# Kernel optimization log

Hardware: AMD Instinct MI355X
Metric: run time of the kernel (lower is better)

The kernel has to match this reference:

```python
import jax, jax.numpy as jnp
import numpy as np
from jax import lax

B, S, D, H = 512, 1024, 24, 64


def setup_inputs() -> dict:
    key = jax.random.key(0)
    ks = jax.random.split(key, 7)
    x = jax.random.normal(ks[0], (B, S, D), dtype=jnp.float32)
    t = jax.random.randint(ks[1], (B,), 0, S, dtype=jnp.int64)
    # Keras GRUCell params (reset_after=True -> bias has shape [2, 3H])
    W = jax.random.normal(ks[2], (D, 3 * H), dtype=jnp.float32) * 0.05   # input kernel
    U = jax.random.normal(ks[3], (H, 3 * H), dtype=jnp.float32) * 0.05   # recurrent kernel
    b = jax.random.normal(ks[4], (2, 3 * H), dtype=jnp.float32) * 0.05   # [input_bias, recurrent_bias]
    Wd = jax.random.normal(ks[5], (H, 1), dtype=jnp.float32) * 0.05      # dense kernel
    bd = jnp.zeros((1,), dtype=jnp.float32)                              # dense bias
    return {"x": x, "t": t, "W": W, "U": U, "b": b, "Wd": Wd, "bd": bd}


def _gru_masked(x, t, W, U, b):
    Bq, Sq, _ = x.shape
    Hq = U.shape[0]
    # prefix mask: True where step index < length (tf.sequence_mask)
    mask = jnp.arange(Sq)[None, :] < t[:, None]          # (B, S) bool
    x_proj = jnp.einsum('bsd,dk->bsk', x, W) + b[0]      # (B, S, 3H) precomputed input gates

    def step(h, inp):
        xp, m = inp                                      # xp: (B, 3H), m: (B,)
        hp = h @ U + b[1]                                # (B, 3H)
        xz, xr, xh = jnp.split(xp, 3, axis=-1)
        hz, hr, hh = jnp.split(hp, 3, axis=-1)
        z = jax.nn.sigmoid(xz + hz)
        r = jax.nn.sigmoid(xr + hr)
        c = jnp.tanh(xh + r * hh)                        # reset_after=True formulation
        h_new = z * h + (1.0 - z) * c
        h_new = jnp.where(m[:, None], h_new, h)          # masked step: carry state/output
        return h_new, h_new

    h0 = jnp.zeros((Bq, Hq), x.dtype)
    xs = jnp.swapaxes(x_proj, 0, 1)                      # (S, B, 3H)
    ms = jnp.swapaxes(mask, 0, 1)                        # (S, B)
    _, hs = lax.scan(step, h0, (xs, ms))
    return jnp.swapaxes(hs, 0, 1)                        # (B, S, H)


def reference(x, t, W, U, b, Wd, bd):
    rnn_out = _gru_masked(x, t, W, U, b)                 # (B, S, H)
    logit = rnn_out @ Wd + bd                            # (B, S, 1)
    return jax.nn.sigmoid(logit)
```

## Files before the change

kernel.cpp:

```cpp
#include <hip/hip_runtime.h>
#include <cstdint>
#include <cstddef>


typedef float  v2f __attribute__((ext_vector_type(2)));
typedef float  v4f __attribute__((ext_vector_type(4)));
typedef _Float16 h2 __attribute__((ext_vector_type(2)));
typedef _Float16 h8 __attribute__((ext_vector_type(8)));

__device__ __forceinline__ float frcp(float x) { return __builtin_amdgcn_rcpf(x); }

#if defined(__has_builtin)
#if __has_builtin(__builtin_amdgcn_fdot2)
#define HAVE_FDOT2 1
#endif
#endif

__device__ __forceinline__ float fdot2(h2 a, h2 b, float acc) {
#ifdef HAVE_FDOT2
    return __builtin_amdgcn_fdot2(a, b, acc, false);
#else
    return fmaf((float)a.x, (float)b.x, fmaf((float)a.y, (float)b.y, acc));
#endif
}

#define PAIR(v8, m) __builtin_shufflevector((v8), (v8), 2*(m), 2*(m)+1)

#define DOT4(acc, Warr, off, v)                              \
    acc = fdot2((Warr)[(off) + 0], PAIR((v), 0), acc);       \
    acc = fdot2((Warr)[(off) + 1], PAIR((v), 1), acc);       \
    acc = fdot2((Warr)[(off) + 2], PAIR((v), 2), acc);       \
    acc = fdot2((Warr)[(off) + 3], PAIR((v), 3), acc);

__global__ __launch_bounds__(64, 1) void gru1_kernel(
    const float* __restrict__ xg,
    const int*   __restrict__ tg,
    const float* __restrict__ Wg,
    const float* __restrict__ Ug,
    const float* __restrict__ bg,
    const float* __restrict__ Wdg,
    const float* __restrict__ bdg,
    float*       __restrict__ outg)
{
    const int b = blockIdx.x;
    const int j = threadIdx.x;

    __shared__ __align__(16) _Float16 h16[64];
    __shared__ __align__(16) _Float16 xbuf[64 * 24];
    __shared__ __align__(16) float    p_lds[64 * 66];
    __shared__ float o_last;

    const int   t    = tg[b];
    float*      outb = outg + (size_t)b * 1024;
    const float bdv  = bdg[0];

    if (t <= 0) {
        const float fill = frcp(1.f + __expf(-bdv));
        for (int i = j; i < 1024; i += 64) outb[i] = fill;
        return;
    }

    h2 Uz[32], Ur[32], Uc[32];
    #pragma unroll
    for (int k = 0; k < 32; ++k) {
        const float* r0 = Ug + (2 * k)     * 192;
        const float* r1 = Ug + (2 * k + 1) * 192;
        Uz[k] = (h2){ (_Float16)(-r0[j]),            (_Float16)(-r1[j]) };
        Ur[k] = (h2){ (_Float16)(-r0[64 + j]),       (_Float16)(-r1[64 + j]) };
        Uc[k] = (h2){ (_Float16)(2.f * r0[128 + j]), (_Float16)(2.f * r1[128 + j]) };
    }
    h2 Wz[12], Wr[12], Wc[12];
    #pragma unroll
    for (int d = 0; d < 12; ++d) {
        const float* r0 = Wg + (2 * d)     * 192;
        const float* r1 = Wg + (2 * d + 1) * 192;
        Wz[d] = (h2){ (_Float16)(-r0[j]),            (_Float16)(-r1[j]) };
        Wr[d] = (h2){ (_Float16)(-r0[64 + j]),       (_Float16)(-r1[64 + j]) };
        Wc[d] = (h2){ (_Float16)(2.f * r0[128 + j]), (_Float16)(2.f * r1[128 + j]) };
    }
    const float bzn  = -(bg[j]      + bg[192 + j]);
    const float brn  = -(bg[64 + j] + bg[256 + j]);
    const float b0c2 = 2.f * bg[128 + j];
    const float b1c2 = 2.f * bg[320 + j];
    const float wdj  = Wdg[j];

    const float* xb = xg + (size_t)b * 24576;

    {
        const v4f* src = (const v4f*)(xb + j * 24);
        v4f g0 = src[0], g1 = src[1], g2 = src[2], g3 = src[3], g4 = src[4], g5 = src[5];
        h8 o0, o1, o2;
        #pragma unroll
        for (int i = 0; i < 4; ++i) {
            o0[i]     = (_Float16)g0[i];  o0[4 + i] = (_Float16)g1[i];
            o1[i]     = (_Float16)g2[i];  o1[4 + i] = (_Float16)g3[i];
            o2[i]     = (_Float16)g4[i];  o2[4 + i] = (_Float16)g5[i];
        }
        h8* dst = (h8*)(xbuf + j * 24);
        dst[0] = o0; dst[1] = o1; dst[2] = o2;
    }
    h16[j] = (_Float16)0.f;

    v4f pf[6];
    if (t > 64) {
        const v4f* ns = (const v4f*)(xb + 1536 + j * 24);
        #pragma unroll
        for (int i = 0; i < 6; ++i) pf[i] = ns[i];
    }

    float hold = 0.f;

    for (int base = 0; base < t; base += 64) {
        const int cnt = (t - base < 64) ? (t - base) : 64;

        if (base > 0) {
            {
                const v2f* pr = (const v2f*)(p_lds + j * 66);
                v2f s2 = (v2f){0.f, 0.f};
                #pragma unroll
                for (int i = 0; i < 32; ++i) s2 += pr[i];
                outb[base - 64 + j] = frcp(1.f + __expf(-(s2.x + s2.y + bdv)));
            }
            {
                h8 o0, o1, o2;
                #pragma unroll
                for (int i = 0; i < 4; ++i) {
                    o0[i]     = (_Float16)pf[0][i];  o0[4 + i] = (_Float16)pf[1][i];
                    o1[i]     = (_Float16)pf[2][i];  o1[4 + i] = (_Float16)pf[3][i];
                    o2[i]     = (_Float16)pf[4][i];  o2[4 + i] = (_Float16)pf[5][i];
                }
                h8* dst = (h8*)(xbuf + j * 24);
                dst[0] = o0; dst[1] = o1; dst[2] = o2;
            }
            if (base + 64 < t) {
                const v4f* ns = (const v4f*)(xb + (size_t)(base + 64) * 24 + j * 24);
                #pragma unroll
                for (int i = 0; i < 6; ++i) pf[i] = ns[i];
            }
        }

        for (int c = 0; c < cnt; ++c) {
            const h8* hp = (const h8*)h16;
            h8 hv[8];
            #pragma unroll
            for (int i = 0; i < 8; ++i) hv[i] = hp[i];
            const h8* xp = (const h8*)(xbuf + c * 24);
            h8 xa = xp[0], xcv = xp[1], xe = xp[2];

            float ran = brn;
            #pragma unroll
            for (int i = 0; i < 8; ++i) { DOT4(ran, Ur, 4 * i, hv[i]); }
            DOT4(ran, Wr, 0, xa); DOT4(ran, Wr, 4, xcv); DOT4(ran, Wr, 8, xe);
            const float er = __expf(ran);

            float zan = bzn;
            #pragma unroll
            for (int i = 0; i < 8; ++i) { DOT4(zan, Uz, 4 * i, hv[i]); }
            DOT4(zan, Wz, 0, xa); DOT4(zan, Wz, 4, xcv); DOT4(zan, Wz, 8, xe);
            const float ez = __expf(zan);

            float ca = b1c2, xca = b0c2;
            #pragma unroll
            for (int i = 0; i < 8; ++i) { DOT4(ca, Uc, 4 * i, hv[i]); }
            DOT4(xca, Wc, 0, xa); DOT4(xca, Wc, 4, xcv); DOT4(xca, Wc, 8, xe);

            const float r  = frcp(1.f + er);
            const float z  = frcp(1.f + ez);
            const float y  = fmaf(r, ca, xca);
            const float cg = 1.f - 2.f * frcp(1.f + __expf(y));
            const float hn = fmaf(z, hold - cg, cg);
            hold = hn;

            h16[j] = (_Float16)hn;
            p_lds[c * 66 + j] = hn * wdj;
        }
    }

    const int lastbase = ((t - 1) >> 6) << 6;
    const int lastcnt  = t - lastbase;
    if (j < lastcnt) {
        const v2f* pr = (const v2f*)(p_lds + j * 66);
        v2f s2 = (v2f){0.f, 0.f};
        #pragma unroll
        for (int i = 0; i < 32; ++i) s2 += pr[i];
        const float o = frcp(1.f + __expf(-(s2.x + s2.y + bdv)));
        outb[lastbase + j] = o;
        if (j == lastcnt - 1) o_last = o;
    }
    const float fill = o_last;
    for (int i = t + j; i < 1024; i += 64) outb[i] = fill;
}

extern "C" void kernel_launch(void* const* d_in, const int* in_sizes, int n_in,
                              void* d_out, int out_size, void* d_ws, size_t ws_size,
                              hipStream_t stream) {
    (void)in_sizes; (void)n_in; (void)d_ws; (void)ws_size; (void)out_size;
    const float* x  = (const float*)d_in[0];
    const int*   t  = (const int*)d_in[1];
    const float* W  = (const float*)d_in[2];
    const float* U  = (const float*)d_in[3];
    const float* bb = (const float*)d_in[4];
    const float* Wd = (const float*)d_in[5];
    const float* bd = (const float*)d_in[6];
    float* out = (float*)d_out;

    hipLaunchKernelGGL(gru1_kernel, dim3(512), dim3(64), 0, stream,
                       x, t, W, U, bb, Wd, bd, out);
}
```

Baseline: 379.1 us.

## Sort sequences by length and process two per block with interleaved steps

A small preliminary kernel ranks the 512 sequence lengths in descending order into a permutation. The main kernel then gives each block a pair of similar-length sequences and runs their GRU recurrences interleaved in one wavefront, falling back to a single-sequence step once the shorter sequence ends. This gives the serial dependency chain two independent streams of dot products and exponentials to hide latency, and halves the block count to 256. The cost is an extra kernel launch, a global sort pass over lengths, and doubled register and LDS use per block.

```diff
diff --git a/kernel.cpp b/kernel.cpp
--- a/kernel.cpp
+++ b/kernel.cpp
@@ -32,7 +32,138 @@
     acc = fdot2((Warr)[(off) + 2], PAIR((v), 2), acc);       \
     acc = fdot2((Warr)[(off) + 3], PAIR((v), 3), acc);
 
-__global__ __launch_bounds__(64, 1) void gru1_kernel(
+__global__ void rank512_kernel(const int* __restrict__ tg, int* __restrict__ perm) {
+    const int i = threadIdx.x;
+    const int ti = tg[i];
+    int rank = 0;
+    for (int k = 0; k < 512; ++k) {
+        const int tk = tg[k];
+        rank += (int)((tk > ti) | ((tk == ti) & (k < i)));
+    }
+    perm[rank] = i;
+}
+
+#define STAGE24(DSTP, SRCP)                                                     \
+  { const v4f* s_ = (const v4f*)(SRCP);                                         \
+    const v4f g0_=s_[0],g1_=s_[1],g2_=s_[2],g3_=s_[3],g4_=s_[4],g5_=s_[5];      \
+    h8 o0_,o1_,o2_;                                                             \
+    _Pragma("unroll")                                                           \
+    for (int i_=0;i_<4;++i_){ o0_[i_]=(_Float16)g0_[i_]; o0_[4+i_]=(_Float16)g1_[i_]; \
+      o1_[i_]=(_Float16)g2_[i_]; o1_[4+i_]=(_Float16)g3_[i_];                   \
+      o2_[i_]=(_Float16)g4_[i_]; o2_[4+i_]=(_Float16)g5_[i_]; }                 \
+    h8* d_=(h8*)(DSTP); d_[0]=o0_; d_[1]=o1_; d_[2]=o2_; }
+
+#define PREFETCH24(PF, SRCP)                                                    \
+  { const v4f* s_=(const v4f*)(SRCP);                                           \
+    _Pragma("unroll") for (int i_=0;i_<6;++i_) (PF)[i_]=s_[i_]; }
+
+#define COMMIT24(DSTP, PF)                                                      \
+  { h8 o0_,o1_,o2_;                                                             \
+    _Pragma("unroll")                                                           \
+    for (int i_=0;i_<4;++i_){ o0_[i_]=(_Float16)(PF)[0][i_]; o0_[4+i_]=(_Float16)(PF)[1][i_]; \
+      o1_[i_]=(_Float16)(PF)[2][i_]; o1_[4+i_]=(_Float16)(PF)[3][i_];           \
+      o2_[i_]=(_Float16)(PF)[4][i_]; o2_[4+i_]=(_Float16)(PF)[5][i_]; }         \
+    h8* d_=(h8*)(DSTP); d_[0]=o0_; d_[1]=o1_; d_[2]=o2_; }
+
+#define REDUCE_CHUNK(S, RBASE, RCNT, TI, OUTB)                                  \
+  if (j < (RCNT)) {                                                             \
+    const v2f* pr_ = (const v2f*)(&p_lds[S][j*66]);                             \
+    v2f a2_ = (v2f){0.f,0.f};                                                   \
+    _Pragma("unroll") for (int i_=0;i_<32;++i_) a2_ += pr_[i_];                 \
+    const float o_ = frcp(1.f + __expf(-(a2_.x + a2_.y + bdv)));                \
+    (OUTB)[(RBASE)+j] = o_;                                                     \
+    if ((RBASE)+j == (TI)-1) olast[S] = o_;                                     \
+  }
+
+#define STEP_A(C)                                                               \
+  { const h8* xp_ = (const h8*)(&xbuf[0][(C)*24]);                              \
+    const h8 xa_=xp_[0], xb_=xp_[1], xc_=xp_[2];                                \
+    const h8* hp_ = (const h8*)(&h16[0][0]);                                    \
+    const h8 h0_=hp_[0],h1_=hp_[1],h2_=hp_[2],h3_=hp_[3],                       \
+             h4_=hp_[4],h5_=hp_[5],h6_=hp_[6],h7_=hp_[7];                       \
+    float ran_=brn, zan_=bzn, xca_=b0c2;                                        \
+    DOT4(ran_,Wr,0,xa_); DOT4(ran_,Wr,4,xb_); DOT4(ran_,Wr,8,xc_);              \
+    DOT4(zan_,Wz,0,xa_); DOT4(zan_,Wz,4,xb_); DOT4(zan_,Wz,8,xc_);              \
+    DOT4(xca_,Wc,0,xa_); DOT4(xca_,Wc,4,xb_); DOT4(xca_,Wc,8,xc_);              \
+    DOT4(ran_,Ur,0,h0_); DOT4(ran_,Ur,4,h1_); DOT4(ran_,Ur,8,h2_);              \
+    DOT4(ran_,Ur,12,h3_); DOT4(ran_,Ur,16,h4_); DOT4(ran_,Ur,20,h5_);           \
+    DOT4(ran_,Ur,24,h6_); DOT4(ran_,Ur,28,h7_);                                 \
+    const float er_ = __expf(ran_);                                             \
+    DOT4(zan_,Uz,0,h0_); DOT4(zan_,Uz,4,h1_); DOT4(zan_,Uz,8,h2_);              \
+    DOT4(zan_,Uz,12,h3_); DOT4(zan_,Uz,16,h4_); DOT4(zan_,Uz,20,h5_);           \
+    DOT4(zan_,Uz,24,h6_); DOT4(zan_,Uz,28,h7_);                                 \
+    const float ez_ = __expf(zan_);                                             \
+    float ca_ = b1c2;                                                           \
+    DOT4(ca_,Uc,0,h0_); DOT4(ca_,Uc,4,h1_); DOT4(ca_,Uc,8,h2_);                 \
+    DOT4(ca_,Uc,12,h3_); DOT4(ca_,Uc,16,h4_); DOT4(ca_,Uc,20,h5_);              \
+    DOT4(ca_,Uc,24,h6_); DOT4(ca_,Uc,28,h7_);                                   \
+    const float r_ = frcp(1.f + er_);                                           \
+    const float z_ = frcp(1.f + ez_);                                           \
+    const float y_ = fmaf(r_, ca_, xca_);                                       \
+    const float cg_ = 1.f - 2.f * frcp(1.f + __expf(y_));                       \
+    const float hn_ = fmaf(z_, holdA - cg_, cg_);                               \
+    holdA = hn_;                                                                \
+    h16[0][j] = (_Float16)hn_;                                                  \
+    p_lds[0][(C)*66+j] = hn_ * wdj;                                             \
+  }
+
+#define DUAL_STEP(C)                                                            \
+  { const h8* xpA_ = (const h8*)(&xbuf[0][(C)*24]);                             \
+    const h8 xaA_=xpA_[0], xbA_=xpA_[1], xcA_=xpA_[2];                          \
+    const h8* xpB_ = (const h8*)(&xbuf[1][(C)*24]);                             \
+    const h8 xaB_=xpB_[0], xbB_=xpB_[1], xcB_=xpB_[2];                          \
+    const h8* hpA_ = (const h8*)(&h16[0][0]);                                   \
+    const h8 hA0_=hpA_[0],hA1_=hpA_[1],hA2_=hpA_[2],hA3_=hpA_[3],               \
+             hA4_=hpA_[4],hA5_=hpA_[5],hA6_=hpA_[6],hA7_=hpA_[7];               \
+    const h8* hpB_ = (const h8*)(&h16[1][0]);                                   \
+    const h8 hB0_=hpB_[0],hB1_=hpB_[1],hB2_=hpB_[2],hB3_=hpB_[3],               \
+             hB4_=hpB_[4],hB5_=hpB_[5],hB6_=hpB_[6],hB7_=hpB_[7];               \
+    float ranA_=brn, zanA_=bzn, xcaA_=b0c2;                                     \
+    float ranB_=brn, zanB_=bzn, xcaB_=b0c2;                                     \
+    DOT4(ranA_,Wr,0,xaA_); DOT4(ranA_,Wr,4,xbA_); DOT4(ranA_,Wr,8,xcA_);        \
+    DOT4(ranB_,Wr,0,xaB_); DOT4(ranB_,Wr,4,xbB_); DOT4(ranB_,Wr,8,xcB_);        \
+    DOT4(zanA_,Wz,0,xaA_); DOT4(zanA_,Wz,4,xbA_); DOT4(zanA_,Wz,8,xcA_);        \
+    DOT4(zanB_,Wz,0,xaB_); DOT4(zanB_,Wz,4,xbB_); DOT4(zanB_,Wz,8,xcB_);        \
+    DOT4(xcaA_,Wc,0,xaA_); DOT4(xcaA_,Wc,4,xbA_); DOT4(xcaA_,Wc,8,xcA_);        \
+    DOT4(xcaB_,Wc,0,xaB_); DOT4(xcaB_,Wc,4,xbB_); DOT4(xcaB_,Wc,8,xcB_);        \
+    DOT4(ranA_,Ur,0,hA0_); DOT4(ranA_,Ur,4,hA1_); DOT4(ranA_,Ur,8,hA2_);        \
+    DOT4(ranA_,Ur,12,hA3_); DOT4(ranA_,Ur,16,hA4_); DOT4(ranA_,Ur,20,hA5_);     \
+    DOT4(ranA_,Ur,24,hA6_); DOT4(ranA_,Ur,28,hA7_);                             \
+    const float erA_ = __expf(ranA_);                                           \
+    DOT4(ranB_,Ur,0,hB0_); DOT4(ranB_,Ur,4,hB1_); DOT4(ranB_,Ur,8,hB2_);        \
+    DOT4(ranB_,Ur,12,hB3_); DOT4(ranB_,Ur,16,hB4_); DOT4(ranB_,Ur,20,hB5_);     \
+    DOT4(ranB_,Ur,24,hB6_); DOT4(ranB_,Ur,28,hB7_);                             \
+    const float erB_ = __expf(ranB_);                                           \
+    DOT4(zanA_,Uz,0,hA0_); DOT4(zanA_,Uz,4,hA1_); DOT4(zanA_,Uz,8,hA2_);        \
+    DOT4(zanA_,Uz,12,hA3_); DOT4(zanA_,Uz,16,hA4_); DOT4(zanA_,Uz,20,hA5_);     \
+    DOT4(zanA_,Uz,24,hA6_); DOT4(zanA_,Uz,28,hA7_);                             \
+    const float ezA_ = __expf(zanA_);                                           \
+    DOT4(zanB_,Uz,0,hB0_); DOT4(zanB_,Uz,4,hB1_); DOT4(zanB_,Uz,8,hB2_);        \
+    DOT4(zanB_,Uz,12,hB3_); DOT4(zanB_,Uz,16,hB4_); DOT4(zanB_,Uz,20,hB5_);     \
+    DOT4(zanB_,Uz,24,hB6_); DOT4(zanB_,Uz,28,hB7_);                             \
+    const float ezB_ = __expf(zanB_);                                           \
+    float caA_ = b1c2;                                                          \
+    DOT4(caA_,Uc,0,hA0_); DOT4(caA_,Uc,4,hA1_); DOT4(caA_,Uc,8,hA2_);           \
+    DOT4(caA_,Uc,12,hA3_); DOT4(caA_,Uc,16,hA4_); DOT4(caA_,Uc,20,hA5_);        \
+    DOT4(caA_,Uc,24,hA6_); DOT4(caA_,Uc,28,hA7_);                               \
+    float caB_ = b1c2;                                                          \
+    DOT4(caB_,Uc,0,hB0_); DOT4(caB_,Uc,4,hB1_); DOT4(caB_,Uc,8,hB2_);           \
+    DOT4(caB_,Uc,12,hB3_); DOT4(caB_,Uc,16,hB4_); DOT4(caB_,Uc,20,hB5_);        \
+    DOT4(caB_,Uc,24,hB6_); DOT4(caB_,Uc,28,hB7_);                               \
+    const float rA_ = frcp(1.f + erA_), zA_ = frcp(1.f + ezA_);                 \
+    const float rB_ = frcp(1.f + erB_), zB_ = frcp(1.f + ezB_);                 \
+    const float yA_ = fmaf(rA_, caA_, xcaA_);                                   \
+    const float yB_ = fmaf(rB_, caB_, xcaB_);                                   \
+    const float cgA_ = 1.f - 2.f * frcp(1.f + __expf(yA_));                     \
+    const float cgB_ = 1.f - 2.f * frcp(1.f + __expf(yB_));                     \
+    const float hnA_ = fmaf(zA_, holdA - cgA_, cgA_);                           \
+    const float hnB_ = fmaf(zB_, holdB - cgB_, cgB_);                           \
+    holdA = hnA_;  holdB = hnB_;                                                \
+    h16[0][j] = (_Float16)hnA_;  h16[1][j] = (_Float16)hnB_;                    \
+    p_lds[0][(C)*66+j] = hnA_ * wdj;  p_lds[1][(C)*66+j] = hnB_ * wdj;          \
+  }
+
+__global__ __launch_bounds__(64, 1) void gru_dual_kernel(
     const float* __restrict__ xg,
     const int*   __restrict__ tg,
     const float* __restrict__ Wg,
@@ -40,23 +171,28 @@
     const float* __restrict__ bg,
     const float* __restrict__ Wdg,
     const float* __restrict__ bdg,
+    const int*   __restrict__ perm,
     float*       __restrict__ outg)
 {
     const int b = blockIdx.x;
     const int j = threadIdx.x;
 
-    __shared__ __align__(16) _Float16 h16[64];
-    __shared__ __align__(16) _Float16 xbuf[64 * 24];
-    __shared__ __align__(16) float    p_lds[64 * 66];
-    __shared__ float o_last;
-
-    const int   t    = tg[b];
-    float*      outb = outg + (size_t)b * 1024;
-    const float bdv  = bdg[0];
-
-    if (t <= 0) {
-        const float fill = frcp(1.f + __expf(-bdv));
-        for (int i = j; i < 1024; i += 64) outb[i] = fill;
+    __shared__ __align__(16) _Float16 h16[2][64];
+    __shared__ __align__(16) _Float16 xbuf[2][64 * 24];
+    __shared__ __align__(16) float    p_lds[2][64 * 66];
+    __shared__ float olast[2];
+
+    const int sA = perm[2 * b];
+    const int sB = perm[2 * b + 1];
+    const int tA = tg[sA];
+    const int tB = tg[sB];
+    float* outA = outg + (size_t)sA * 1024;
+    float* outB = outg + (size_t)sB * 1024;
+    const float bdv = bdg[0];
+    const float sbd = frcp(1.f + __expf(-bdv));
+
+    if (tA <= 0) {
+        for (int i = j; i < 1024; i += 64) { outA[i] = sbd; outB[i] = sbd; }
         return;
     }
 
@@ -84,117 +220,56 @@
     const float b1c2 = 2.f * bg[320 + j];
     const float wdj  = Wdg[j];
 
-    const float* xb = xg + (size_t)b * 24576;
-
-    {
-        const v4f* src = (const v4f*)(xb + j * 24);
-        v4f g0 = src[0], g1 = src[1], g2 = src[2], g3 = src[3], g4 = src[4], g5 = src[5];
-        h8 o0, o1, o2;
-        #pragma unroll
-        for (int i = 0; i < 4; ++i) {
-            o0[i]     = (_Float16)g0[i];  o0[4 + i] = (_Float16)g1[i];
-            o1[i]     = (_Float16)g2[i];  o1[4 + i] = (_Float16)g3[i];
-            o2[i]     = (_Float16)g4[i];  o2[4 + i] = (_Float16)g5[i];
+    const float* xbA = xg + (size_t)sA * 24576;
+    const float* xbB = xg + (size_t)sB * 24576;
+
+    STAGE24(&xbuf[0][j * 24], xbA + j * 24);
+    if (tB > 0) STAGE24(&xbuf[1][j * 24], xbB + j * 24);
+    h16[0][j] = (_Float16)0.f;
+    h16[1][j] = (_Float16)0.f;
+
+    v4f pfA[6], pfB[6];
+    if (tA > 64) PREFETCH24(pfA, xbA + 1536 + j * 24);
+    if (tB > 64) PREFETCH24(pfB, xbB + 1536 + j * 24);
+
+    float holdA = 0.f, holdB = 0.f;
+
+    for (int base = 0; base < tA; base += 64) {
+        const int  cnt  = (tA - base < 64) ? (tA - base) : 64;
+        const bool dual = base < tB;
+
+        if (base > 0) {
+            const int rbase = base - 64;
+            REDUCE_CHUNK(0, rbase, 64, tA, outA);
+            if (rbase < tB) { REDUCE_CHUNK(1, rbase, 64, tB, outB); }
+            COMMIT24(&xbuf[0][j * 24], pfA);
+            if (dual) COMMIT24(&xbuf[1][j * 24], pfB);
+            if (base + 64 < tA) PREFETCH24(pfA, xbA + (size_t)(base + 64) * 24 + j * 24);
+            if (base + 64 < tB) PREFETCH24(pfB, xbB + (size_t)(base + 64) * 24 + j * 24);
         }
-        h8* dst = (h8*)(xbuf + j * 24);
-        dst[0] = o0; dst[1] = o1; dst[2] = o2;
-    }
-    h16[j] = (_Float16)0.f;
-
-    v4f pf[6];
-    if (t > 64) {
-        const v4f* ns = (const v4f*)(xb + 1536 + j * 24);
-        #pragma unroll
-        for (int i = 0; i < 6; ++i) pf[i] = ns[i];
-    }
-
-    float hold = 0.f;
-
-    for (int base = 0; base < t; base += 64) {
-        const int cnt = (t - base < 64) ? (t - base) : 64;
-
-        if (base > 0) {
-            {
-                const v2f* pr = (const v2f*)(p_lds + j * 66);
-                v2f s2 = (v2f){0.f, 0.f};
-                #pragma unroll
-                for (int i = 0; i < 32; ++i) s2 += pr[i];
-                outb[base - 64 + j] = frcp(1.f + __expf(-(s2.x + s2.y + bdv)));
-            }
-            {
-                h8 o0, o1, o2;
-                #pragma unroll
-                for (int i = 0; i < 4; ++i) {
-                    o0[i]     = (_Float16)pf[0][i];  o0[4 + i] = (_Float16)pf[1][i];
-                    o1[i]     = (_Float16)pf[2][i];  o1[4 + i] = (_Float16)pf[3][i];
-                    o2[i]     = (_Float16)pf[4][i];  o2[4 + i] = (_Float16)pf[5][i];
-                }
-                h8* dst = (h8*)(xbuf + j * 24);
-                dst[0] = o0; dst[1] = o1; dst[2] = o2;
-            }
-            if (base + 64 < t) {
-                const v4f* ns = (const v4f*)(xb + (size_t)(base + 64) * 24 + j * 24);
-                #pragma unroll
-                for (int i = 0; i < 6; ++i) pf[i] = ns[i];
-            }
+
+        if (dual) {
+            for (int c = 0; c < cnt; ++c) { DUAL_STEP(c); }
+        } else {
+            for (int c = 0; c < cnt; ++c) { STEP_A(c); }
         }
-
-        for (int c = 0; c < cnt; ++c) {
-            const h8* hp = (const h8*)h16;
-            h8 hv[8];
-            #pragma unroll
-            for (int i = 0; i < 8; ++i) hv[i] = hp[i];
-            const h8* xp = (const h8*)(xbuf + c * 24);
-            h8 xa = xp[0], xcv = xp[1], xe = xp[2];
-
-            float ran = brn;
-            #pragma unroll
-            for (int i = 0; i < 8; ++i) { DOT4(ran, Ur, 4 * i, hv[i]); }
-            DOT4(ran, Wr, 0, xa); DOT4(ran, Wr, 4, xcv); DOT4(ran, Wr, 8, xe);
-            const float er = __expf(ran);
-
-            float zan = bzn;
-            #pragma unroll
-            for (int i = 0; i < 8; ++i) { DOT4(zan, Uz, 4 * i, hv[i]); }
-            DOT4(zan, Wz, 0, xa); DOT4(zan, Wz, 4, xcv); DOT4(zan, Wz, 8, xe);
-            const float ez = __expf(zan);
-
-            float ca = b1c2, xca = b0c2;
-            #pragma unroll
-            for (int i = 0; i < 8; ++i) { DOT4(ca, Uc, 4 * i, hv[i]); }
-            DOT4(xca, Wc, 0, xa); DOT4(xca, Wc, 4, xcv); DOT4(xca, Wc, 8, xe);
-
-            const float r  = frcp(1.f + er);
-            const float z  = frcp(1.f + ez);
-            const float y  = fmaf(r, ca, xca);
-            const float cg = 1.f - 2.f * frcp(1.f + __expf(y));
-            const float hn = fmaf(z, hold - cg, cg);
-            hold = hn;
-
-            h16[j] = (_Float16)hn;
-            p_lds[c * 66 + j] = hn * wdj;
-        }
-    }
-
-    const int lastbase = ((t - 1) >> 6) << 6;
-    const int lastcnt  = t - lastbase;
-    if (j < lastcnt) {
-        const v2f* pr = (const v2f*)(p_lds + j * 66);
-        v2f s2 = (v2f){0.f, 0.f};
-        #pragma unroll
-        for (int i = 0; i < 32; ++i) s2 += pr[i];
-        const float o = frcp(1.f + __expf(-(s2.x + s2.y + bdv)));
-        outb[lastbase + j] = o;
-        if (j == lastcnt - 1) o_last = o;
-    }
-    const float fill = o_last;
-    for (int i = t + j; i < 1024; i += 64) outb[i] = fill;
+    }
+
+    const int lastbase = ((tA - 1) >> 6) << 6;
+    const int lastcnt  = tA - lastbase;
+    REDUCE_CHUNK(0, lastbase, lastcnt, tA, outA);
+    if (lastbase < tB) { REDUCE_CHUNK(1, lastbase, lastcnt, tB, outB); }
+
+    const float fillA = olast[0];
+    const float fillB = (tB > 0) ? olast[1] : sbd;
+    for (int i = tA + j; i < 1024; i += 64) outA[i] = fillA;
+    for (int i = tB + j; i < 1024; i += 64) outB[i] = fillB;
 }
 
 extern "C" void kernel_launch(void* const* d_in, const int* in_sizes, int n_in,
                               void* d_out, int out_size, void* d_ws, size_t ws_size,
                               hipStream_t stream) {
-    (void)in_sizes; (void)n_in; (void)d_ws; (void)ws_size; (void)out_size;
+    (void)in_sizes; (void)n_in; (void)ws_size; (void)out_size;
     const float* x  = (const float*)d_in[0];
     const int*   t  = (const int*)d_in[1];
     const float* W  = (const float*)d_in[2];
@@ -203,7 +278,9 @@
     const float* Wd = (const float*)d_in[5];
     const float* bd = (const float*)d_in[6];
     float* out = (float*)d_out;
-
-    hipLaunchKernelGGL(gru1_kernel, dim3(512), dim3(64), 0, stream,
-                       x, t, W, U, bb, Wd, bd, out);
-}
+    int*   perm = (int*)d_ws;
+
+    hipLaunchKernelGGL(rank512_kernel, dim3(1), dim3(512), 0, stream, t, perm);
+    hipLaunchKernelGGL(gru_dual_kernel, dim3(256), dim3(64), 0, stream,
+                       x, t, W, U, bb, Wd, bd, perm, out);
+}
```

Result: slower. 702.5 us (+85.3%).
